# Performance work log

Measured on AMD Instinct MI355X. Metric: run time of the kernel, lower is better.

The kernel has to match this reference:

```python
import jax, jax.numpy as jnp
import numpy as np

DROPOUT_P = 0.1
EMBED = 128  # head dim; inv_scale_factor = sqrt(EMBED)


def setup_inputs() -> dict:
    key = jax.random.key(0)
    ks = jax.random.split(key, 9)
    B, S, H, D = 4, 2048, 16, EMBED
    mk = lambda k, shape: jax.random.normal(k, shape, dtype=jnp.float32)
    return {
        "query": mk(ks[0], (B, S, H, D)),
        "key": mk(ks[1], (B, S, H, D)),
        "value": mk(ks[2], (B, S, H, D)),
        "Wq": mk(ks[3], (D, D)) / np.sqrt(D),
        "bq": mk(ks[4], (D,)) * 0.01,
        "Wk": mk(ks[5], (D, D)) / np.sqrt(D),
        "bk": mk(ks[6], (D,)) * 0.01,
        "Wv": mk(ks[7], (D, D)) / np.sqrt(D),
        "bv": mk(ks[8], (D,)) * 0.01,
    }


def reference(query, key, value, Wq, bq, Wk, bk, Wv, bv):
    # Linear (torch convention: x @ W.T + b) then permute(0,2,1,3): [B,S,H,D] -> [B,H,S,D]
    q = (query @ Wq.T + bq).transpose(0, 2, 1, 3)
    k = (key @ Wk.T + bk).transpose(0, 2, 1, 3)
    v = (value @ Wv.T + bv).transpose(0, 2, 1, 3)
    scale = 1.0 / jnp.sqrt(jnp.float32(EMBED))  # div by embed_size**0.5
    scores = jnp.einsum("bhqd,bhkd->bhqk", q, k) * scale
    probs = jax.nn.softmax(scores, axis=-1)
    # deterministic inverted dropout with fixed key (train-mode dropout)
    keep = jax.random.bernoulli(jax.random.key(42), 1.0 - DROPOUT_P, probs.shape)
    probs = jnp.where(keep, probs / (1.0 - DROPOUT_P), 0.0)
    return jnp.einsum("bhqk,bhkd->bhqd", probs, v)
```

## Files before the change

kernel.cpp:

```cpp
#include <hip/hip_runtime.h>
#include <stdint.h>

#define BB 4
#define SS 2048
#define HH 16
#define DD 128

typedef __attribute__((ext_vector_type(8))) short bf16x8;
typedef __attribute__((ext_vector_type(4))) float f32x4;

__device__ __forceinline__ float bf2f(uint16_t u) {
  union { uint32_t i; float f; } x; x.i = ((uint32_t)u) << 16; return x.f;
}
__device__ __forceinline__ uint16_t f2bf(float f) {
  union { float f; uint32_t i; } u; u.f = f;
  uint32_t r = u.i + 0x7FFFu + ((u.i >> 16) & 1u);
  return (uint16_t)(r >> 16);
}

#define TF_C 3865470464u
#define TF_ROUND(r) { x0 += x1; x1 = __builtin_amdgcn_alignbit(x1, x1, 32 - (r)) ^ x0; }

__device__ __forceinline__ void tf2x32(uint32_t k0, uint32_t k1, uint32_t c0, uint32_t c1,
                                       uint32_t& o0, uint32_t& o1) {
  const uint32_t k2 = 0x1BD11BDAu ^ k0 ^ k1;
  uint32_t x0 = c0 + k0, x1 = c1 + k1;
  TF_ROUND(13) TF_ROUND(15) TF_ROUND(26) TF_ROUND(6)
  x0 += k1; x1 += k2 + 1u;
  TF_ROUND(17) TF_ROUND(29) TF_ROUND(16) TF_ROUND(24)
  x0 += k2; x1 += k0 + 2u;
  TF_ROUND(13) TF_ROUND(15) TF_ROUND(26) TF_ROUND(6)
  x0 += k0; x1 += k1 + 3u;
  TF_ROUND(17) TF_ROUND(29) TF_ROUND(16) TF_ROUND(24)
  x0 += k1; x1 += k2 + 4u;
  TF_ROUND(13) TF_ROUND(15) TF_ROUND(26) TF_ROUND(6)
  x0 += k2; x1 += k0 + 5u;
  o0 = x0; o1 = x1;
}

__device__ __forceinline__ uint32_t tf_bit_part(uint32_t i) {
  uint32_t o0, o1;
  tf2x32(0u, 42u, 0u, i, o0, o1);
  return ((o0 ^ o1) < TF_C) ? 1u : 0u;
}

__global__ void detect_kernel(const uint16_t* __restrict__ q, int* __restrict__ flag) {
  if (blockIdx.x == 0 && threadIdx.x == 0) {
    int ok = 1;
    for (int i = 0; i < 64; ++i) {
      float a = fabsf(bf2f(q[2 * i]));
      if (!(a == 0.0f || (a > 9.0e-13f && a < 64.0f))) ok = 0;
    }
    *flag = ok;
  }
}

__global__ __launch_bounds__(256) void mask_kernel(unsigned long long* __restrict__ mask) {
  const int lane = threadIdx.x & 63;
  const uint32_t wid = ((uint32_t)blockIdx.x * 256u + (uint32_t)threadIdx.x) >> 6;
  const uint32_t base = wid * 256u;
  unsigned long long b[4];
#pragma unroll
  for (int u = 0; u < 4; ++u) {
    uint32_t i = base + (uint32_t)(u * 64 + lane);
    uint32_t o0, o1;
    tf2x32(0u, 42u, 0u, i, o0, o1);
    b[u] = __ballot((o0 ^ o1) < TF_C);
  }
  if (lane == 0) {
    uint32_t w = base >> 6;
#pragma unroll
    for (int u = 0; u < 4; ++u) mask[w + u] = b[u];
  }
}

__global__ __launch_bounds__(256) void proj_kernel(
    const void* __restrict__ xq, const void* __restrict__ xk, const void* __restrict__ xv,
    const void* __restrict__ Wq, const void* __restrict__ bq,
    const void* __restrict__ Wk, const void* __restrict__ bk,
    const void* __restrict__ Wv, const void* __restrict__ bv,
    uint16_t* __restrict__ Qo, uint16_t* __restrict__ Ko, uint16_t* __restrict__ Vo,
    const int* __restrict__ flag) {
  const int isbf = *flag;
  const int tz = blockIdx.y;
  const void* x = (tz == 0) ? xq : (tz == 1) ? xk : xv;
  const void* W = (tz == 0) ? Wq : (tz == 1) ? Wk : Wv;
  const void* bs = (tz == 0) ? bq : (tz == 1) ? bk : bv;
  uint16_t* out = (tz == 0) ? Qo : (tz == 1) ? Ko : Vo;
  const int vtrans = (tz == 2);

  const int wave = threadIdx.x >> 6, lane = threadIdx.x & 63;
  const int c = lane & 15, quad = lane >> 4;
  const int m0 = blockIdx.x * 64 + wave * 16;
  const int mrow = m0 + c;

  bf16x8 af[4];
  if (isbf) {
    const uint16_t* xr = (const uint16_t*)x + (size_t)mrow * DD + quad * 8;
#pragma unroll
    for (int t = 0; t < 4; ++t) af[t] = *(const bf16x8*)(xr + t * 32);
  } else {
    const float* xr = (const float*)x + (size_t)mrow * DD + quad * 8;
#pragma unroll
    for (int t = 0; t < 4; ++t) {
#pragma unroll
      for (int j = 0; j < 8; ++j) af[t][j] = (short)f2bf(xr[t * 32 + j]);
    }
  }

  size_t obase[4];
#pragma unroll
  for (int r = 0; r < 4; ++r) {
    int m = m0 + quad * 4 + r;
    int b = m >> 15;
    int s = (m >> 4) & (SS - 1);
    int h = m & (HH - 1);
    obase[r] = vtrans ? ((size_t)(b * HH + h) * SS * DD + (size_t)(s >> 5) * (DD * 32) + (s & 31))
                      : (((size_t)(b * HH + h) * SS + (size_t)s) * DD);
  }

  for (int nt = 0; nt < 8; ++nt) {
    f32x4 acc = {0.f, 0.f, 0.f, 0.f};
    const int n = nt * 16 + c;
    if (isbf) {
      const uint16_t* wr = (const uint16_t*)W + (size_t)n * DD + quad * 8;
#pragma unroll
      for (int t = 0; t < 4; ++t)
        acc = __builtin_amdgcn_mfma_f32_16x16x32_bf16(af[t], *(const bf16x8*)(wr + t * 32), acc, 0, 0, 0);
    } else {
      const float* wr = (const float*)W + (size_t)n * DD + quad * 8;
#pragma unroll
      for (int t = 0; t < 4; ++t) {
        bf16x8 bfr;
#pragma unroll
        for (int j = 0; j < 8; ++j) bfr[j] = (short)f2bf(wr[t * 32 + j]);
        acc = __builtin_amdgcn_mfma_f32_16x16x32_bf16(af[t], bfr, acc, 0, 0, 0);
      }
    }
    const float bias = isbf ? bf2f(((const uint16_t*)bs)[n]) : ((const float*)bs)[n];
#pragma unroll
    for (int r = 0; r < 4; ++r) {
      float v = acc[r] + bias;
      size_t o = obase[r] + (vtrans ? (size_t)n * 32 : (size_t)n);
      out[o] = f2bf(v);
    }
  }
}

__global__ __launch_bounds__(256) void attn_kernel(
    const uint16_t* __restrict__ Q, const uint16_t* __restrict__ K, const uint16_t* __restrict__ Vt,
    const uint32_t* __restrict__ mask32, void* __restrict__ outv, const int* __restrict__ flag) {
  __shared__ __align__(16) uint16_t Ks[2][32][128];
  __shared__ __align__(16) uint16_t Vs[2][128][32];
  __shared__ __align__(16) uint16_t pl[4][16][40];
  const int isbf = *flag;
  const int tid = threadIdx.x;
  const int wave = tid >> 6, lane = tid & 63;
  const int c = lane & 15, quad = lane >> 4;
  const int bh = blockIdx.x >> 5;
  const int q0 = (blockIdx.x & 31) * 64 + wave * 16;

  const uint16_t* Qb = Q + (size_t)bh * SS * DD;
  const uint16_t* Kb = K + (size_t)bh * SS * DD;
  const uint16_t* Vb = Vt + (size_t)bh * SS * DD;

  bf16x8 qf[4];
  {
    const uint16_t* qr = Qb + (q0 + c) * DD + quad * 8;
#pragma unroll
    for (int t = 0; t < 4; ++t) qf[t] = *(const bf16x8*)(qr + t * 32);
  }

  const f32x4 zero = {0.f, 0.f, 0.f, 0.f};
  f32x4 o[8];
#pragma unroll
  for (int i = 0; i < 8; ++i) o[i] = zero;
  float lsum[4] = {0.f, 0.f, 0.f, 0.f};

  const float sc2 = 0.12751744f;

  uint32_t mb[4];
#pragma unroll
  for (int r = 0; r < 4; ++r)
    mb[r] = ((uint32_t)bh * SS + (uint32_t)(q0 + quad * 4 + r)) * (SS / 32);

  uint16_t(*plw)[40] = pl[wave];

  const int krow = tid >> 4;
  const int kd0 = krow * 256 + (((tid & 15) * 16) ^ ((krow & 7) << 4));
  const int kd1 = kd0 + 16 * 256;
  const int vd0 = tid * 16, vd1 = vd0 + 4096;
  const uint16_t* kga = Kb + krow * DD + (tid & 15) * 8;
  const uint16_t* vga = Vb + tid * 8;

  bf16x8 ksa = *(const bf16x8*)(kga);
  bf16x8 ksb = *(const bf16x8*)(kga + 16 * DD);
  bf16x8 vsa = *(const bf16x8*)(vga);
  bf16x8 vsb = *(const bf16x8*)(vga + 2048);
  {
    char* kd = (char*)Ks[0]; *(bf16x8*)(kd + kd0) = ksa; *(bf16x8*)(kd + kd1) = ksb;
    char* vd = (char*)Vs[0]; *(bf16x8*)(vd + vd0) = vsa; *(bf16x8*)(vd + vd1) = vsb;
  }
  __syncthreads();

  const int ksw = (c & 7) << 4;
  int cur = 0;

  for (int kt = 0; kt < SS / 32; ++kt) {
    const int ktn = (kt + 1) & 63;
    ksa = *(const bf16x8*)(kga + ktn * 32 * DD);
    ksb = *(const bf16x8*)(kga + ktn * 32 * DD + 16 * DD);
    vsa = *(const bf16x8*)(vga + ktn * 4096);
    vsb = *(const bf16x8*)(vga + ktn * 4096 + 2048);

    const char* klds = (const char*)Ks[cur];
    f32x4 sf[2];
#pragma unroll
    for (int ks = 0; ks < 2; ++ks) {
      f32x4 acc = zero;
      const char* kr = klds + (ks * 16 + c) * 256;
#pragma unroll
      for (int t = 0; t < 4; ++t) {
        bf16x8 kf = *(const bf16x8*)(kr + ((quad * 16 + t * 64) ^ ksw));
        acc = __builtin_amdgcn_mfma_f32_16x16x32_bf16(qf[t], kf, acc, 0, 0, 0);
      }
      sf[ks] = acc;
    }
    uint32_t mw[4];
#pragma unroll
    for (int r = 0; r < 4; ++r) mw[r] = mask32[mb[r] + kt];
#pragma unroll
    for (int ks = 0; ks < 2; ++ks) {
#pragma unroll
      for (int r = 0; r < 4; ++r) {
        float p = __builtin_amdgcn_exp2f(sf[ks][r] * sc2);
        lsum[r] += p;
        float pm = ((mw[r] >> (ks * 16 + c)) & 1u) ? p : 0.0f;
        plw[quad * 4 + r][ks * 16 + c] = f2bf(pm);
      }
    }
    bf16x8 pa = *(const bf16x8*)(&plw[c][quad * 8]);
    const char* vlds = (const char*)Vs[cur] + c * 64 + quad * 16;
#pragma unroll
    for (int dt = 0; dt < 8; ++dt) {
      bf16x8 vf = *(const bf16x8*)(vlds + dt * 1024);
      o[dt] = __builtin_amdgcn_mfma_f32_16x16x32_bf16(pa, vf, o[dt], 0, 0, 0);
    }

    {
      char* kd = (char*)Ks[cur ^ 1]; *(bf16x8*)(kd + kd0) = ksa; *(bf16x8*)(kd + kd1) = ksb;
      char* vd = (char*)Vs[cur ^ 1]; *(bf16x8*)(vd + vd0) = vsa; *(bf16x8*)(vd + vd1) = vsb;
    }
    __syncthreads();
    cur ^= 1;
  }

#pragma unroll
  for (int r = 0; r < 4; ++r) {
    float v = lsum[r];
    v += __shfl_xor(v, 1);
    v += __shfl_xor(v, 2);
    v += __shfl_xor(v, 4);
    v += __shfl_xor(v, 8);
    lsum[r] = 1.0f / (0.9f * v);
  }

  const size_t ob = (size_t)bh * SS * DD;
  if (isbf) {
    uint16_t* outp = (uint16_t*)outv;
#pragma unroll
    for (int dt = 0; dt < 8; ++dt)
#pragma unroll
      for (int r = 0; r < 4; ++r)
        outp[ob + (size_t)(q0 + quad * 4 + r) * DD + dt * 16 + c] = f2bf(o[dt][r] * lsum[r]);
  } else {
    float* outp = (float*)outv;
#pragma unroll
    for (int dt = 0; dt < 8; ++dt)
#pragma unroll
      for (int r = 0; r < 4; ++r)
        outp[ob + (size_t)(q0 + quad * 4 + r) * DD + dt * 16 + c] = o[dt][r] * lsum[r];
  }

  if (blockIdx.x == 0 && wave == 0) {
    uint32_t o0, o1;
    tf2x32(0u, 0u, 0u, 0u, o0, o1);
    bool bad1 = (o0 != 0x6b200159u) || (o1 != 0x99ba4efeu);
    uint32_t cnt = (uint32_t)lane * 1928377u + 77777u;
    uint32_t bit0 = (mask32[cnt >> 5] >> (cnt & 31)) & 1u;
    bool bad2 = (tf_bit_part(cnt) != bit0);
#pragma unroll
    for (int ks = 0; ks < 2; ++ks)
#pragma unroll
      for (int r = 0; r < 4; ++r)
        plw[quad * 4 + r][ks * 16 + c] = f2bf((float)((quad * 4 + r) * 32 + ks * 16 + c));
    bf16x8 tp = *(const bf16x8*)(&plw[c][quad * 8]);
    bool bad3 = false;
#pragma unroll
    for (int j = 0; j < 8; ++j)
      bad3 |= ((uint16_t)tp[j] != f2bf((float)(c * 32 + quad * 8 + j)));
    bf16x8 ta, tb;
#pragma unroll
    for (int j = 0; j < 8; ++j) {
      ta[j] = (short)f2bf((float)(c * 32 + quad * 8 + j));
      tb[j] = (short)((quad * 8 + j == c) ? f2bf(1.0f) : 0);
    }
    f32x4 tc = zero;
    tc = __builtin_amdgcn_mfma_f32_16x16x32_bf16(ta, tb, tc, 0, 0, 0);
    bool bad4 = false;
#pragma unroll
    for (int r = 0; r < 4; ++r)
      bad4 |= (tc[r] != bf2f(f2bf((float)((quad * 4 + r) * 32 + c))));
#pragma unroll
    for (int j = 0; j < 8; ++j) {
      ta[j] = (short)((quad * 8 + j == c) ? f2bf(1.0f) : 0);
      tb[j] = (short)f2bf((float)(c * 32 + quad * 8 + j));
    }
    f32x4 td = zero;
    td = __builtin_amdgcn_mfma_f32_16x16x32_bf16(ta, tb, td, 0, 0, 0);
    bool bad5 = false;
#pragma unroll
    for (int r = 0; r < 4; ++r)
      bad5 |= (td[r] != bf2f(f2bf((float)(c * 32 + quad * 4 + r))));
    float main_d0 = __shfl(o[0][0] * lsum[0], 0);
    float main_d64 = __shfl(o[4][0] * lsum[0], 0);
    float a0 = 0.f, a64 = 0.f, al = 0.f;
    for (int k = lane; k < SS; k += 64) {
      float s = 0.f;
      for (int d = 0; d < DD; ++d) s += bf2f(Qb[d]) * bf2f(Kb[k * DD + d]);
      float p = __builtin_amdgcn_exp2f(s * sc2);
      al += p;
      if ((mask32[k >> 5] >> (k & 31)) & 1u) {
        a0 += p * bf2f(Vb[(size_t)(k >> 5) * 4096 + (k & 31)]);
        a64 += p * bf2f(Vb[(size_t)(k >> 5) * 4096 + 64 * 32 + (k & 31)]);
      }
    }
#pragma unroll
    for (int off = 32; off; off >>= 1) {
      a0 += __shfl_xor(a0, off);
      a64 += __shfl_xor(a64, off);
      al += __shfl_xor(al, off);
    }
    bool bad6 = (fabsf(a0 / (0.9f * al) - main_d0) > 0.02f) ||
                (fabsf(a64 / (0.9f * al) - main_d64) > 0.02f);

    unsigned long long m1 = __ballot(bad1), m2 = __ballot(bad2), m3 = __ballot(bad3),
                       m4 = __ballot(bad4), m5 = __ballot(bad5), m6 = __ballot(bad6);
    if (lane == 0) {
      float s = 0.f;
      if (m1) s = 1e8f;
      else if (m2) s = 1e7f;
      else if (m3) s = 1e6f;
      else if (m4) s = 1e5f;
      else if (m5) s = 4e4f;
      else if (m6) s = 2e4f;
      if (s != 0.f) {
        if (isbf) ((uint16_t*)outv)[0] = f2bf(s);
        else ((float*)outv)[0] = s;
      }
    }
  }
}

extern "C" void kernel_launch(void* const* d_in, const int* in_sizes, int n_in,
                              void* d_out, int out_size, void* d_ws, size_t ws_size,
                              hipStream_t stream) {
  char* ws = (char*)d_ws;
  int* flag = (int*)ws;
  uint16_t* Qo = (uint16_t*)(ws + 256);
  uint16_t* Ko = Qo + (size_t)BB * HH * SS * DD;
  uint16_t* Vo = Ko + (size_t)BB * HH * SS * DD;
  unsigned long long* mask = (unsigned long long*)(ws + 256 + 3ull * BB * HH * SS * DD * 2ull);

  hipLaunchKernelGGL(detect_kernel, dim3(1), dim3(64), 0, stream,
                     (const uint16_t*)d_in[0], flag);
  hipLaunchKernelGGL(mask_kernel, dim3(262144), dim3(256), 0, stream, mask);
  hipLaunchKernelGGL(proj_kernel, dim3(2048, 3), dim3(256), 0, stream,
                     d_in[0], d_in[1], d_in[2], d_in[3], d_in[4], d_in[5], d_in[6], d_in[7], d_in[8],
                     Qo, Ko, Vo, flag);
  hipLaunchKernelGGL(attn_kernel, dim3(2048), dim3(256), 0, stream,
                     Qo, Ko, Vo, (const uint32_t*)mask, d_out, flag);
}
```

Before: 1.116 ms.

## Generate dropout mask inline in attention kernel instead of precomputed bitmask

Removes the separate mask kernel, which ran threefry over all B*H*S*S elements and wrote a 32 MB bitmask. The attention kernel now evaluates threefry per probability element while computing softmax. This trades global mask writes and reads for extra ALU work inside the attention loop. It also sets a launch-bounds occupancy hint of 4 blocks and drops the mask consistency self-check.

```diff
diff --git a/kernel.cpp b/kernel.cpp
--- a/kernel.cpp
+++ b/kernel.cpp
@@ -55,25 +55,6 @@
   }
 }
 
-__global__ __launch_bounds__(256) void mask_kernel(unsigned long long* __restrict__ mask) {
-  const int lane = threadIdx.x & 63;
-  const uint32_t wid = ((uint32_t)blockIdx.x * 256u + (uint32_t)threadIdx.x) >> 6;
-  const uint32_t base = wid * 256u;
-  unsigned long long b[4];
-#pragma unroll
-  for (int u = 0; u < 4; ++u) {
-    uint32_t i = base + (uint32_t)(u * 64 + lane);
-    uint32_t o0, o1;
-    tf2x32(0u, 42u, 0u, i, o0, o1);
-    b[u] = __ballot((o0 ^ o1) < TF_C);
-  }
-  if (lane == 0) {
-    uint32_t w = base >> 6;
-#pragma unroll
-    for (int u = 0; u < 4; ++u) mask[w + u] = b[u];
-  }
-}
-
 __global__ __launch_bounds__(256) void proj_kernel(
     const void* __restrict__ xq, const void* __restrict__ xk, const void* __restrict__ xv,
     const void* __restrict__ Wq, const void* __restrict__ bq,
@@ -147,9 +128,9 @@
   }
 }
 
-__global__ __launch_bounds__(256) void attn_kernel(
+__global__ __launch_bounds__(256, 4) void attn_kernel(
     const uint16_t* __restrict__ Q, const uint16_t* __restrict__ K, const uint16_t* __restrict__ Vt,
-    const uint32_t* __restrict__ mask32, void* __restrict__ outv, const int* __restrict__ flag) {
+    void* __restrict__ outv, const int* __restrict__ flag) {
   __shared__ __align__(16) uint16_t Ks[2][32][128];
   __shared__ __align__(16) uint16_t Vs[2][128][32];
   __shared__ __align__(16) uint16_t pl[4][16][40];
@@ -179,10 +160,10 @@
 
   const float sc2 = 0.12751744f;
 
-  uint32_t mb[4];
+  uint32_t ibase[4];
 #pragma unroll
   for (int r = 0; r < 4; ++r)
-    mb[r] = ((uint32_t)bh * SS + (uint32_t)(q0 + quad * 4 + r)) * (SS / 32);
+    ibase[r] = ((uint32_t)bh * SS + (uint32_t)(q0 + quad * 4 + r)) * SS + (uint32_t)c;
 
   uint16_t(*plw)[40] = pl[wave];
 
@@ -226,16 +207,16 @@
       }
       sf[ks] = acc;
     }
-    uint32_t mw[4];
-#pragma unroll
-    for (int r = 0; r < 4; ++r) mw[r] = mask32[mb[r] + kt];
+    const uint32_t ik = (uint32_t)kt * 32u;
 #pragma unroll
     for (int ks = 0; ks < 2; ++ks) {
 #pragma unroll
       for (int r = 0; r < 4; ++r) {
         float p = __builtin_amdgcn_exp2f(sf[ks][r] * sc2);
         lsum[r] += p;
-        float pm = ((mw[r] >> (ks * 16 + c)) & 1u) ? p : 0.0f;
+        uint32_t b0, b1;
+        tf2x32(0u, 42u, 0u, ibase[r] + ik + (uint32_t)(ks * 16), b0, b1);
+        float pm = ((b0 ^ b1) < TF_C) ? p : 0.0f;
         plw[quad * 4 + r][ks * 16 + c] = f2bf(pm);
       }
     }
@@ -286,9 +267,6 @@
     uint32_t o0, o1;
     tf2x32(0u, 0u, 0u, 0u, o0, o1);
     bool bad1 = (o0 != 0x6b200159u) || (o1 != 0x99ba4efeu);
-    uint32_t cnt = (uint32_t)lane * 1928377u + 77777u;
-    uint32_t bit0 = (mask32[cnt >> 5] >> (cnt & 31)) & 1u;
-    bool bad2 = (tf_bit_part(cnt) != bit0);
 #pragma unroll
     for (int ks = 0; ks < 2; ++ks)
 #pragma unroll
@@ -330,7 +308,7 @@
       for (int d = 0; d < DD; ++d) s += bf2f(Qb[d]) * bf2f(Kb[k * DD + d]);
       float p = __builtin_amdgcn_exp2f(s * sc2);
       al += p;
-      if ((mask32[k >> 5] >> (k & 31)) & 1u) {
+      if (tf_bit_part((uint32_t)k)) {
         a0 += p * bf2f(Vb[(size_t)(k >> 5) * 4096 + (k & 31)]);
         a64 += p * bf2f(Vb[(size_t)(k >> 5) * 4096 + 64 * 32 + (k & 31)]);
       }
@@ -344,12 +322,11 @@
     bool bad6 = (fabsf(a0 / (0.9f * al) - main_d0) > 0.02f) ||
                 (fabsf(a64 / (0.9f * al) - main_d64) > 0.02f);
 
-    unsigned long long m1 = __ballot(bad1), m2 = __ballot(bad2), m3 = __ballot(bad3),
+    unsigned long long m1 = __ballot(bad1), m3 = __ballot(bad3),
                        m4 = __ballot(bad4), m5 = __ballot(bad5), m6 = __ballot(bad6);
     if (lane == 0) {
       float s = 0.f;
       if (m1) s = 1e8f;
-      else if (m2) s = 1e7f;
       else if (m3) s = 1e6f;
       else if (m4) s = 1e5f;
       else if (m5) s = 4e4f;
@@ -370,14 +347,12 @@
   uint16_t* Qo = (uint16_t*)(ws + 256);
   uint16_t* Ko = Qo + (size_t)BB * HH * SS * DD;
   uint16_t* Vo = Ko + (size_t)BB * HH * SS * DD;
-  unsigned long long* mask = (unsigned long long*)(ws + 256 + 3ull * BB * HH * SS * DD * 2ull);
 
   hipLaunchKernelGGL(detect_kernel, dim3(1), dim3(64), 0, stream,
                      (const uint16_t*)d_in[0], flag);
-  hipLaunchKernelGGL(mask_kernel, dim3(262144), dim3(256), 0, stream, mask);
   hipLaunchKernelGGL(proj_kernel, dim3(2048, 3), dim3(256), 0, stream,
                      d_in[0], d_in[1], d_in[2], d_in[3], d_in[4], d_in[5], d_in[6], d_in[7], d_in[8],
                      Qo, Ko, Vo, flag);
   hipLaunchKernelGGL(attn_kernel, dim3(2048), dim3(256), 0, stream,
-                     Qo, Ko, Vo, (const uint32_t*)mask, d_out, flag);
-}
+                     Qo, Ko, Vo, d_out, flag);
+}
```

Measured after the change: 1.152 ms. +3.2%, slower.
